# Performance work log

Hardware: AMD Instinct MI355X
Metric: run time of the kernel (lower is better)

## Reference

```python
import jax, jax.numpy as jnp
import numpy as np

B, C, H, W = 16384, 1, 2048, 1
HID = 5


def setup_inputs() -> dict:
    key = jax.random.key(0)
    kx, kl, k1, k2, k3, k4 = jax.random.split(key, 6)
    x = jax.random.normal(kx, (B, C, H, W), dtype=jnp.float32)
    # random ragged lengths in [1, H]; zero out padded tail so the module's
    # (x != 0).any(dim=2) mask recovers exactly these lengths
    lengths = jax.random.randint(kl, (B,), 1, H + 1)
    t_idx = jnp.arange(H)
    valid = (t_idx[None, :] < lengths[:, None])  # [B, H]
    x = x * valid[:, None, :, None].astype(jnp.float32)
    s = 1.0 / np.sqrt(HID)
    W_ih = jax.random.uniform(k1, (4 * HID, 1), minval=-s, maxval=s, dtype=jnp.float32)
    W_hh = jax.random.uniform(k2, (4 * HID, HID), minval=-s, maxval=s, dtype=jnp.float32)
    b_ih = jax.random.uniform(k3, (4 * HID,), minval=-s, maxval=s, dtype=jnp.float32)
    b_hh = jax.random.uniform(k4, (4 * HID,), minval=-s, maxval=s, dtype=jnp.float32)
    return {"x": x, "W_ih": W_ih, "W_hh": W_hh, "b_ih": b_ih, "b_hh": b_hh}


def reference(x, W_ih, W_hh, b_ih, b_hh):
    b, c, h, w = x.shape
    feats = c * w  # == 1 (LSTM input_size)
    xr = x.reshape(b, h, feats)  # [B, T, 1]
    mask = jnp.any(xr != 0, axis=2)  # [B, T]
    lengths = mask.sum(axis=1).astype(jnp.int32)  # [B]

    bias = b_ih + b_hh  # [4H]
    # precompute input projection for all timesteps: [B, T, 4H]
    x_proj = jnp.einsum('btf,gf->btg', xr, W_ih) + bias
    xs = jnp.moveaxis(x_proj, 1, 0)  # [T, B, 4H]

    h0 = jnp.zeros((b, HID), dtype=x.dtype)
    c0 = jnp.zeros((b, HID), dtype=x.dtype)

    def step(carry, inp):
        hp, cp = carry
        xg, t = inp
        gates = xg + hp @ W_hh.T  # [B, 4H]
        i, f, g, o = jnp.split(gates, 4, axis=1)
        i = jax.nn.sigmoid(i)
        f = jax.nn.sigmoid(f)
        g = jnp.tanh(g)
        o = jax.nn.sigmoid(o)
        cn = f * cp + i * g
        hn = o * jnp.tanh(cn)
        # packed semantics: only advance state while t < length (per sample)
        upd = (t < lengths)[:, None]
        hn = jnp.where(upd, hn, hp)
        cn = jnp.where(upd, cn, cp)
        return (hn, cn), None

    (hT, cT), _ = jax.lax.scan(step, (h0, c0), (xs, jnp.arange(h)))
    return hT[None]  # [1, B, HID] matching torch h shape
```

## Files before the change

kernel.cpp:

```cpp
#include <hip/hip_runtime.h>

#define Bn    16384
#define Tn    2048
#define HIDn  5
#define NBINS 2048

static __device__ __forceinline__ float rcp_fast(float v) {
    return __builtin_amdgcn_rcpf(v);
}
static __device__ __forceinline__ float exp2_fast(float v) {
    return __builtin_amdgcn_exp2f(v);
}

template <int K>
static __device__ __forceinline__ float bcast8(float v) {
    return __int_as_float(
        __builtin_amdgcn_ds_swizzle(__float_as_int(v), (K << 5) | 0x18));
}
template <int K>
static __device__ __forceinline__ int bcast8i(int v) {
    return __builtin_amdgcn_ds_swizzle(v, (K << 5) | 0x18);
}

__global__ __launch_bounds__(256) void len_kernel(const float* __restrict__ x,
                                                  int* __restrict__ lengths) {
    const int gtid = blockIdx.x * 256 + threadIdx.x;
    const int row  = gtid >> 6;
    const int lane = threadIdx.x & 63;
    const float4* r = reinterpret_cast<const float4*>(x + (size_t)row * Tn);
    int cnt = 0;
    #pragma unroll
    for (int i = 0; i < Tn / 4 / 64; ++i) {
        float4 v = r[i * 64 + lane];
        cnt += (v.x != 0.0f) + (v.y != 0.0f) + (v.z != 0.0f) + (v.w != 0.0f);
    }
    #pragma unroll
    for (int off = 32; off > 0; off >>= 1) cnt += __shfl_xor(cnt, off, 64);
    if (lane == 0) lengths[row] = cnt;
}

__global__ __launch_bounds__(1024) void sort_kernel(const int* __restrict__ lengths,
                                                    int* __restrict__ perm,
                                                    int* __restrict__ ctr) {
    __shared__ int bins[NBINS];
    __shared__ int bsum[1024];
    const int tid = threadIdx.x;
    bins[tid] = 0;
    bins[tid + 1024] = 0;
    if (tid == 0) *ctr = 0;
    __syncthreads();
    for (int i = tid; i < Bn; i += 1024) {
        int d = NBINS - lengths[i];
        d = max(0, min(NBINS - 1, d));
        atomicAdd(&bins[d], 1);
    }
    __syncthreads();
    const int a0 = bins[2 * tid], a1 = bins[2 * tid + 1];
    const int s = a0 + a1;
    bsum[tid] = s;
    __syncthreads();
    int acc = s;
    for (int off = 1; off < 1024; off <<= 1) {
        int v = (tid >= off) ? bsum[tid - off] : 0;
        __syncthreads();
        acc += v;
        bsum[tid] = acc;
        __syncthreads();
    }
    const int excl = acc - s;
    bins[2 * tid]     = excl;
    bins[2 * tid + 1] = excl + a0;
    __syncthreads();
    for (int i = tid; i < Bn; i += 1024) {
        int d = NBINS - lengths[i];
        d = max(0, min(NBINS - 1, d));
        const int p = atomicAdd(&bins[d], 1);
        perm[p] = i;
    }
}

__global__ __launch_bounds__(256, 2) void lstm_kernel(const float* __restrict__ x,
                                                      const float* __restrict__ Wih,
                                                      const float* __restrict__ Whh,
                                                      const float* __restrict__ bih,
                                                      const float* __restrict__ bhh,
                                                      const int* __restrict__ lengths,
                                                      const int* __restrict__ perm,
                                                      int* __restrict__ ctr,
                                                      float* __restrict__ out) {
    const int lsub = threadIdx.x & 7;
    const int k    = min(lsub, 4);

    const float L2E   = 1.4426950408889634f;
    const float NL2E2 = -2.0f * L2E;

    float wih[4], bias[4], whh[4][HIDn];
    #pragma unroll
    for (int j = 0; j < 4; ++j) {
        const int   gi = 5 * j + k;
        const float sj = (j == 2) ? NL2E2 : -L2E;
        wih[j]  = Wih[gi] * sj;
        bias[j] = (bih[gi] + bhh[gi]) * sj;
        #pragma unroll
        for (int kk = 0; kk < HIDn; ++kk) whh[j][kk] = Whh[gi * HIDn + kk] * sj;
    }

    bool dead = false, have = false;
    int  b = 0, len = 0, t = 0;
    const float* xrow = x;
    float h0 = 0, h1 = 0, h2 = 0, h3 = 0, h4 = 0;
    float h_own = 0, c = 0;
    float4 xq = make_float4(0.f, 0.f, 0.f, 0.f);

    while (__any(!dead)) {
        if (!dead && t >= len) {
            if (have && lsub < HIDn) out[(size_t)b * HIDn + lsub] = h_own;
            int pos = 0;
            if (lsub == 0) pos = atomicAdd(ctr, 1);
            pos = bcast8i<0>(pos);
            if (pos < Bn) {
                b    = perm[pos];
                len  = lengths[b];
                xrow = x + (size_t)b * Tn;
                t = 0; c = 0; h_own = 0;
                h0 = h1 = h2 = h3 = h4 = 0;
                xq = *reinterpret_cast<const float4*>(xrow);
                have = true;
            } else {
                dead = true; have = false; len = 0;
            }
        }
        if (!dead) {
            const float4 xn = *reinterpret_cast<const float4*>(xrow + min(t + 4, Tn - 4));
            const float xs[4] = { xq.x, xq.y, xq.z, xq.w };
            #pragma unroll
            for (int s = 0; s < 4; ++s) {
                if (t + s < len) {
                    const float xv = xs[s];
                    float p[4];
                    #pragma unroll
                    for (int j = 0; j < 4; ++j) {
                        float pp = fmaf(xv, wih[j], bias[j]);
                        pp = fmaf(h0, whh[j][0], pp);
                        pp = fmaf(h1, whh[j][1], pp);
                        pp = fmaf(h2, whh[j][2], pp);
                        pp = fmaf(h3, whh[j][3], pp);
                        pp = fmaf(h4, whh[j][4], pp);
                        p[j] = pp;
                    }
                    const float x0 = 1.0f + exp2_fast(p[0]);
                    const float x1 = 1.0f + exp2_fast(p[1]);
                    const float x2 = 1.0f + exp2_fast(p[2]);
                    const float x3 = 1.0f + exp2_fast(p[3]);
                    const float r01 = rcp_fast(x0 * x1);
                    const float r23 = rcp_fast(x2 * x3);
                    const float gi_ = x1 * r01;
                    const float gf_ = x0 * r01;
                    const float gg_ = fmaf(2.0f, x3 * r23, -1.0f);
                    const float go_ = x2 * r23;

                    c = fmaf(gf_, c, gi_ * gg_);

                    const float th = fmaf(2.0f, rcp_fast(1.0f + exp2_fast(c * NL2E2)), -1.0f);
                    h_own = go_ * th;

                    h0 = bcast8<0>(h_own);
                    h1 = bcast8<1>(h_own);
                    h2 = bcast8<2>(h_own);
                    h3 = bcast8<3>(h_own);
                    h4 = bcast8<4>(h_own);
                }
            }
            xq = xn;
            t += 4;
        }
    }
}

extern "C" void kernel_launch(void* const* d_in, const int* in_sizes, int n_in,
                              void* d_out, int out_size, void* d_ws, size_t ws_size,
                              hipStream_t stream) {
    const float* x   = (const float*)d_in[0];
    const float* Wih = (const float*)d_in[1];
    const float* Whh = (const float*)d_in[2];
    const float* bih = (const float*)d_in[3];
    const float* bhh = (const float*)d_in[4];
    float* out = (float*)d_out;

    int* lengths = (int*)d_ws;
    int* perm    = lengths + Bn;
    int* ctr     = perm + Bn;

    len_kernel<<<Bn / 4, 256, 0, stream>>>(x, lengths);
    sort_kernel<<<1, 1024, 0, stream>>>(lengths, perm, ctr);
    lstm_kernel<<<Bn * 8 / 256, 256, 0, stream>>>(x, Wih, Whh, bih, bhh,
                                                  lengths, perm, ctr, out);
}
```

Measured before the change: 581.8 us.

## Static row assignment, packed-math gates and rational tanh activations in LSTM

Drops the atomic work queue: each 8-lane group now processes exactly one row, taken from the sorted permutation, and the loop is predicated instead of refilling groups. The length histogram moves into the length kernel through global atomics, with a small zeroing kernel added, so the single-block sort only does the prefix scan and scatter. Gate pre-activations are computed with packed two-wide float vectors. Sigmoid and tanh use a clamped rational (Padé-style) tanh approximation instead of exp2 plus reciprocal. This trims per-step ALU and transcendental work, at the cost of an approximation error near the clamp range and no more dynamic load balancing.

```diff
diff --git a/kernel.cpp b/kernel.cpp
--- a/kernel.cpp
+++ b/kernel.cpp
@@ -5,11 +5,13 @@
 #define HIDn  5
 #define NBINS 2048
 
+typedef float v2f __attribute__((ext_vector_type(2)));
+
 static __device__ __forceinline__ float rcp_fast(float v) {
     return __builtin_amdgcn_rcpf(v);
 }
-static __device__ __forceinline__ float exp2_fast(float v) {
-    return __builtin_amdgcn_exp2f(v);
+static __device__ __forceinline__ float med3(float x, float lo, float hi) {
+    return __builtin_amdgcn_fmed3f(x, lo, hi);
 }
 
 template <int K>
@@ -17,13 +19,14 @@
     return __int_as_float(
         __builtin_amdgcn_ds_swizzle(__float_as_int(v), (K << 5) | 0x18));
 }
-template <int K>
-static __device__ __forceinline__ int bcast8i(int v) {
-    return __builtin_amdgcn_ds_swizzle(v, (K << 5) | 0x18);
+
+__global__ void zero_kernel(int* __restrict__ gbins) {
+    gbins[blockIdx.x * 256 + threadIdx.x] = 0;
 }
 
 __global__ __launch_bounds__(256) void len_kernel(const float* __restrict__ x,
-                                                  int* __restrict__ lengths) {
+                                                  int* __restrict__ lengths,
+                                                  int* __restrict__ gbins) {
     const int gtid = blockIdx.x * 256 + threadIdx.x;
     const int row  = gtid >> 6;
     const int lane = threadIdx.x & 63;
@@ -36,24 +39,21 @@
     }
     #pragma unroll
     for (int off = 32; off > 0; off >>= 1) cnt += __shfl_xor(cnt, off, 64);
-    if (lane == 0) lengths[row] = cnt;
+    if (lane == 0) {
+        lengths[row] = cnt;
+        const int d = max(0, min(NBINS - 1, NBINS - cnt));
+        atomicAdd(&gbins[d], 1);
+    }
 }
 
 __global__ __launch_bounds__(1024) void sort_kernel(const int* __restrict__ lengths,
-                                                    int* __restrict__ perm,
-                                                    int* __restrict__ ctr) {
+                                                    const int* __restrict__ gbins,
+                                                    int* __restrict__ perm) {
     __shared__ int bins[NBINS];
     __shared__ int bsum[1024];
     const int tid = threadIdx.x;
-    bins[tid] = 0;
-    bins[tid + 1024] = 0;
-    if (tid == 0) *ctr = 0;
-    __syncthreads();
-    for (int i = tid; i < Bn; i += 1024) {
-        int d = NBINS - lengths[i];
-        d = max(0, min(NBINS - 1, d));
-        atomicAdd(&bins[d], 1);
-    }
+    bins[tid]        = gbins[tid];
+    bins[tid + 1024] = gbins[tid + 1024];
     __syncthreads();
     const int a0 = bins[2 * tid], a1 = bins[2 * tid + 1];
     const int s = a0 + a1;
@@ -86,95 +86,88 @@
                                                       const float* __restrict__ bhh,
                                                       const int* __restrict__ lengths,
                                                       const int* __restrict__ perm,
-                                                      int* __restrict__ ctr,
                                                       float* __restrict__ out) {
+    const int gtid = blockIdx.x * 256 + threadIdx.x;
+    const int grp  = gtid >> 3;
     const int lsub = threadIdx.x & 7;
     const int k    = min(lsub, 4);
 
-    const float L2E   = 1.4426950408889634f;
-    const float NL2E2 = -2.0f * L2E;
+    const int b   = perm[grp];
+    const int len = lengths[b];
 
-    float wih[4], bias[4], whh[4][HIDn];
-    #pragma unroll
-    for (int j = 0; j < 4; ++j) {
-        const int   gi = 5 * j + k;
-        const float sj = (j == 2) ? NL2E2 : -L2E;
-        wih[j]  = Wih[gi] * sj;
-        bias[j] = (bih[gi] + bhh[gi]) * sj;
+    v2f wihA, wihB, bA, bB, whhA[HIDn], whhB[HIDn];
+    {
+        const int gi = k, gf = 5 + k, gg = 10 + k, go = 15 + k;
+        wihA = (v2f){ Wih[gi] * 0.5f, Wih[gf] * 0.5f };
+        wihB = (v2f){ Wih[gg],        Wih[go] * 0.5f };
+        bA   = (v2f){ (bih[gi] + bhh[gi]) * 0.5f, (bih[gf] + bhh[gf]) * 0.5f };
+        bB   = (v2f){ (bih[gg] + bhh[gg]),        (bih[go] + bhh[go]) * 0.5f };
         #pragma unroll
-        for (int kk = 0; kk < HIDn; ++kk) whh[j][kk] = Whh[gi * HIDn + kk] * sj;
+        for (int kk = 0; kk < HIDn; ++kk) {
+            whhA[kk] = (v2f){ Whh[gi * HIDn + kk] * 0.5f, Whh[gf * HIDn + kk] * 0.5f };
+            whhB[kk] = (v2f){ Whh[gg * HIDn + kk],        Whh[go * HIDn + kk] * 0.5f };
+        }
     }
 
-    bool dead = false, have = false;
-    int  b = 0, len = 0, t = 0;
-    const float* xrow = x;
+    const float* xrow = x + (size_t)b * Tn;
     float h0 = 0, h1 = 0, h2 = 0, h3 = 0, h4 = 0;
-    float h_own = 0, c = 0;
-    float4 xq = make_float4(0.f, 0.f, 0.f, 0.f);
+    float hq = 0, c = 0;
 
-    while (__any(!dead)) {
-        if (!dead && t >= len) {
-            if (have && lsub < HIDn) out[(size_t)b * HIDn + lsub] = h_own;
-            int pos = 0;
-            if (lsub == 0) pos = atomicAdd(ctr, 1);
-            pos = bcast8i<0>(pos);
-            if (pos < Bn) {
-                b    = perm[pos];
-                len  = lengths[b];
-                xrow = x + (size_t)b * Tn;
-                t = 0; c = 0; h_own = 0;
-                h0 = h1 = h2 = h3 = h4 = 0;
-                xq = *reinterpret_cast<const float4*>(xrow);
-                have = true;
-            } else {
-                dead = true; have = false; len = 0;
-            }
+    float4 xq = *reinterpret_cast<const float4*>(xrow);
+    for (int t = 0; __any(t < len); t += 4) {
+        const float4 xn = *reinterpret_cast<const float4*>(xrow + min(t + 4, Tn - 4));
+        const float xs[4] = { xq.x, xq.y, xq.z, xq.w };
+        #pragma unroll
+        for (int s = 0; s < 4; ++s) {
+            const float xv = xs[s];
+            v2f pA = xv * wihA + bA;
+            v2f pB = xv * wihB + bB;
+            pA = h0 * whhA[0] + pA;  pB = h0 * whhB[0] + pB;
+            pA = h1 * whhA[1] + pA;  pB = h1 * whhB[1] + pB;
+            pA = h2 * whhA[2] + pA;  pB = h2 * whhB[2] + pB;
+            pA = h3 * whhA[3] + pA;  pB = h3 * whhB[3] + pB;
+            pA = h4 * whhA[4] + pA;  pB = h4 * whhB[4] + pB;
+            v2f tA, tB;
+            tA.x = med3(pA.x, -4.0f, 4.0f);  tA.y = med3(pA.y, -4.0f, 4.0f);
+            tB.x = med3(pB.x, -4.0f, 4.0f);  tB.y = med3(pB.y, -4.0f, 4.0f);
+            const v2f zA = tA * tA, zB = tB * tB;
+            const v2f nA = (zA * 21.0f + 1260.0f) * zA + 10395.0f;
+            const v2f nB = (zB * 21.0f + 1260.0f) * zB + 10395.0f;
+            const v2f dA = ((zA + 210.0f) * zA + 4725.0f) * zA + 10395.0f;
+            const v2f dB = ((zB + 210.0f) * zB + 4725.0f) * zB + 10395.0f;
+            const float rA = rcp_fast(dA.x * dA.y);
+            const float rB = rcp_fast(dB.x * dB.y);
+            const v2f pnA = tA * nA, pnB = tB * nB;
+            const float ti = (pnA.x * dA.y) * rA;
+            const float tf = (pnA.y * dA.x) * rA;
+            const float tg = (pnB.x * dB.y) * rB;
+            const float to = (pnB.y * dB.x) * rB;
+            const float gi_ = fmaf(ti, 0.5f, 0.5f);
+            const float gf_ = fmaf(tf, 0.5f, 0.5f);
+            const float oo  = fmaf(to, 0.5f, 0.5f);
+
+            const float cn = fmaf(gf_, c, gi_ * tg);
+
+            const float tc = med3(cn, -4.0f, 4.0f);
+            const float zc = tc * tc;
+            const float nc = fmaf(zc, fmaf(zc, 21.0f, 1260.0f), 10395.0f);
+            const float dc = fmaf(zc, fmaf(zc, zc + 210.0f, 4725.0f), 10395.0f);
+            const float hn = (tc * nc) * (oo * rcp_fast(dc));
+
+            const bool upd = (t + s) < len;
+            c  = upd ? cn : c;
+            hq = upd ? hn : hq;
+
+            h0 = bcast8<0>(hq);
+            h1 = bcast8<1>(hq);
+            h2 = bcast8<2>(hq);
+            h3 = bcast8<3>(hq);
+            h4 = bcast8<4>(hq);
         }
-        if (!dead) {
-            const float4 xn = *reinterpret_cast<const float4*>(xrow + min(t + 4, Tn - 4));
-            const float xs[4] = { xq.x, xq.y, xq.z, xq.w };
-            #pragma unroll
-            for (int s = 0; s < 4; ++s) {
-                if (t + s < len) {
-                    const float xv = xs[s];
-                    float p[4];
-                    #pragma unroll
-                    for (int j = 0; j < 4; ++j) {
-                        float pp = fmaf(xv, wih[j], bias[j]);
-                        pp = fmaf(h0, whh[j][0], pp);
-                        pp = fmaf(h1, whh[j][1], pp);
-                        pp = fmaf(h2, whh[j][2], pp);
-                        pp = fmaf(h3, whh[j][3], pp);
-                        pp = fmaf(h4, whh[j][4], pp);
-                        p[j] = pp;
-                    }
-                    const float x0 = 1.0f + exp2_fast(p[0]);
-                    const float x1 = 1.0f + exp2_fast(p[1]);
-                    const float x2 = 1.0f + exp2_fast(p[2]);
-                    const float x3 = 1.0f + exp2_fast(p[3]);
-                    const float r01 = rcp_fast(x0 * x1);
-                    const float r23 = rcp_fast(x2 * x3);
-                    const float gi_ = x1 * r01;
-                    const float gf_ = x0 * r01;
-                    const float gg_ = fmaf(2.0f, x3 * r23, -1.0f);
-                    const float go_ = x2 * r23;
+        xq = xn;
+    }
 
-                    c = fmaf(gf_, c, gi_ * gg_);
-
-                    const float th = fmaf(2.0f, rcp_fast(1.0f + exp2_fast(c * NL2E2)), -1.0f);
-                    h_own = go_ * th;
-
-                    h0 = bcast8<0>(h_own);
-                    h1 = bcast8<1>(h_own);
-                    h2 = bcast8<2>(h_own);
-                    h3 = bcast8<3>(h_own);
-                    h4 = bcast8<4>(h_own);
-                }
-            }
-            xq = xn;
-            t += 4;
-        }
-    }
+    if (lsub < HIDn) out[(size_t)b * HIDn + lsub] = hq;
 }
 
 extern "C" void kernel_launch(void* const* d_in, const int* in_sizes, int n_in,
@@ -189,10 +182,11 @@
 
     int* lengths = (int*)d_ws;
     int* perm    = lengths + Bn;
-    int* ctr     = perm + Bn;
+    int* gbins   = perm + Bn;
 
-    len_kernel<<<Bn / 4, 256, 0, stream>>>(x, lengths);
-    sort_kernel<<<1, 1024, 0, stream>>>(lengths, perm, ctr);
+    zero_kernel<<<NBINS / 256, 256, 0, stream>>>(gbins);
+    len_kernel<<<Bn / 4, 256, 0, stream>>>(x, lengths, gbins);
+    sort_kernel<<<1, 1024, 0, stream>>>(lengths, gbins, perm);
     lstm_kernel<<<Bn * 8 / 256, 256, 0, stream>>>(x, Wih, Whh, bih, bhh,
-                                                  lengths, perm, ctr, out);
+                                                  lengths, perm, out);
 }
```

After: 573.0 us. About the same (-1.5%).
